# Optimization experiments

Measured on AMD Instinct MI355X. Metric: run time of the kernel, lower is better.

The kernel has to match this reference:

```python
import jax, jax.numpy as jnp
import numpy as np

N_NODES = 50000
N_EDGES = 800000
IN_FEAT = 256
OUT_FEAT = 128
P_EDGE = 0.2   # edge dropout rate
P_NODE = 0.1   # node-feature dropout rate
BN_EPS = 1e-5


def setup_inputs() -> dict:
    key = jax.random.key(0)
    ks = jax.random.split(key, 8)
    features = jax.random.normal(ks[0], (N_NODES, IN_FEAT), dtype=jnp.float32)
    W = jax.random.normal(ks[1], (IN_FEAT, OUT_FEAT), dtype=jnp.float32) / np.sqrt(IN_FEAT)
    b = jnp.zeros((OUT_FEAT,), dtype=jnp.float32)
    gamma = jnp.ones((OUT_FEAT,), dtype=jnp.float32)
    beta = jnp.zeros((OUT_FEAT,), dtype=jnp.float32)
    src = jax.random.randint(ks[2], (N_EDGES,), 0, N_NODES, dtype=jnp.int64)
    dst = jax.random.randint(ks[3], (N_EDGES,), 0, N_NODES, dtype=jnp.int64)
    edge_rand = jax.random.uniform(ks[4], (N_EDGES,), dtype=jnp.float32)
    node_rand = jax.random.uniform(ks[5], (N_NODES, OUT_FEAT), dtype=jnp.float32)
    return {"features": features, "W": W, "b": b, "gamma": gamma, "beta": beta,
            "src": src, "dst": dst, "edge_rand": edge_rand, "node_rand": node_rand}


def reference(features, W, b, gamma, beta, src, dst, edge_rand, node_rand):
    dt = features.dtype
    # --- edge dropout: keep-mask over edges (no rescale, per DropEdge convention) ---
    emask = (edge_rand >= P_EDGE).astype(dt)                      # [E]
    # --- GCN conv, norm='both' on the dropped graph ---
    h = features @ W                                              # [N, out] (W first: out < in)
    deg_src = jax.ops.segment_sum(emask, src, num_segments=N_NODES)  # out-degrees
    deg_dst = jax.ops.segment_sum(emask, dst, num_segments=N_NODES)  # in-degrees
    coef = emask * jax.lax.rsqrt(jnp.maximum(deg_src[src], 1.0) * jnp.maximum(deg_dst[dst], 1.0))
    msg = h[src] * coef[:, None]                                  # [E, out]
    agg = jax.ops.segment_sum(msg, dst, num_segments=N_NODES) + b  # [N, out]
    # --- BatchNorm1d (training mode: batch statistics over nodes) ---
    mean = jnp.mean(agg, axis=0)
    var = jnp.var(agg, axis=0)
    y = (agg - mean) * jax.lax.rsqrt(var + BN_EPS) * gamma + beta
    # --- node-feature dropout (inverted scaling) ---
    nmask = (node_rand >= P_NODE).astype(dt) / (1.0 - P_NODE)
    return y * nmask
```

## Files before the change

kernel.cpp:

```cpp
#include <hip/hip_runtime.h>

#define N_NODES 50000
#define N_EDGES 800000
#define IN_FEAT 256
#define OUT_FEAT 128
#define P_EDGE 0.2f
#define P_NODE 0.1f
#define BN_EPS 1e-5f
#define CAP 64
#define NPART 8
#define PART_N 6250
#define ECHUNKS 128
#define CHUNK_E 6250
#define GEMM_BLOCKS 782
#define ZERO_BLOCKS 98
#define PREPW_BLOCKS 128
#define AGG_BLOCKS 1024
#define FIN_BLOCKS 8

typedef __bf16 bf16x8 __attribute__((ext_vector_type(8)));
typedef float floatx4 __attribute__((ext_vector_type(4)));

__device__ inline float bflo(unsigned u) { return __uint_as_float(u << 16); }
__device__ inline float bfhi(unsigned u) { return __uint_as_float(u & 0xffff0000u); }

__global__ __launch_bounds__(256) void k_init(const float* __restrict__ W,
    uint4* __restrict__ zero_base, __bf16* __restrict__ Wt) {
  if (blockIdx.x < ZERO_BLOCKS) {
    int i = blockIdx.x * 256 + threadIdx.x;
    if (i < 25000) zero_base[i] = make_uint4(0u, 0u, 0u, 0u);
  } else {
    int idx = (blockIdx.x - ZERO_BLOCKS) * 256 + threadIdx.x;
    int k = idx >> 7, n = idx & 127;
    Wt[n * IN_FEAT + k] = (__bf16)W[idx];
  }
}

__global__ __launch_bounds__(256) void k_edge(const int* __restrict__ src,
    const int* __restrict__ dst, const float* __restrict__ er,
    unsigned* __restrict__ deg_src, unsigned* __restrict__ deg_dst,
    unsigned short* __restrict__ edge_src) {
  const int part = blockIdx.x & (NPART - 1);
  const int chunk = blockIdx.x >> 3;
  const int nlo = part * PART_N;
  const int nhi = nlo + PART_N;
  const int e0 = chunk * CHUNK_E;
  for (int e = e0 + threadIdx.x; e < e0 + CHUNK_E; e += 256) {
    if (er[e] >= P_EDGE) {
      int s = src[e], d = dst[e];
      if (s >= nlo && s < nhi) atomicAdd(&deg_src[s], 1u);
      if (d >= nlo && d < nhi) {
        unsigned p = atomicAdd(&deg_dst[d], 1u);
        if (p < CAP) edge_src[(unsigned)d * CAP + p] = (unsigned short)s;
      }
    }
  }
}

__device__ inline bf16x8 cvt8(float4 a, float4 b) {
  bf16x8 v;
  v[0] = (__bf16)a.x; v[1] = (__bf16)a.y; v[2] = (__bf16)a.z; v[3] = (__bf16)a.w;
  v[4] = (__bf16)b.x; v[5] = (__bf16)b.y; v[6] = (__bf16)b.z; v[7] = (__bf16)b.w;
  return v;
}

__global__ __launch_bounds__(256) void k_gemm(const float* __restrict__ feat,
    const __bf16* __restrict__ Wt, const unsigned* __restrict__ deg_src,
    __bf16* __restrict__ h) {
  const int lane = threadIdx.x & 63;
  const int wave = threadIdx.x >> 6;
  const int l16 = lane & 15;
  const int quad = lane >> 4;
  const int m0 = blockIdx.x * 64 + wave * 16;

  int mload = m0 + l16;
  if (mload >= N_NODES) mload = N_NODES - 1;

  bf16x8 a[8];
#pragma unroll
  for (int kk = 0; kk < 8; kk++) {
    const float4* p = (const float4*)(feat + (size_t)mload * IN_FEAT + kk * 32 + quad * 8);
    float4 f0 = p[0];
    float4 f1 = p[1];
    a[kk] = cvt8(f0, f1);
  }

  floatx4 acc[8];
#pragma unroll
  for (int g = 0; g < 8; g++) {
    const __bf16* wrow = Wt + (size_t)(g * 16 + l16) * IN_FEAT + quad * 8;
    floatx4 c = {0.f, 0.f, 0.f, 0.f};
#pragma unroll
    for (int kk = 0; kk < 8; kk++) {
      bf16x8 b = *(const bf16x8*)(wrow + kk * 32);
      c = __builtin_amdgcn_mfma_f32_16x16x32_bf16(a[kk], b, c, 0, 0, 0);
    }
    acc[g] = c;
  }

  const int rbase = m0 + quad * 4;
  float s[4];
#pragma unroll
  for (int r = 0; r < 4; r++) {
    int row = rbase + r;
    unsigned dg = (row < N_NODES) ? deg_src[row] : 1u;
    s[r] = rsqrtf((float)(dg ? dg : 1u));
  }
#pragma unroll
  for (int g = 0; g < 8; g++) {
#pragma unroll
    for (int r = 0; r < 4; r++) {
      int row = rbase + r;
      if (row < N_NODES)
        h[(size_t)row * OUT_FEAT + g * 16 + l16] = (__bf16)(acc[g][r] * s[r]);
    }
  }
}

__global__ __launch_bounds__(256) void k_agg(const unsigned short* __restrict__ h,
    const unsigned short* __restrict__ edge_src,
    const unsigned* __restrict__ deg_dst, const float* __restrict__ bias,
    float* __restrict__ out, float* __restrict__ psum, float* __restrict__ pssq) {
  const int wid = threadIdx.x >> 6;
  const int lane = threadIdx.x & 63;
  const int g = lane >> 4;
  const int cl = lane & 15;
  const int wave_global = blockIdx.x * 4 + wid;

  float b8[8];
#pragma unroll
  for (int j = 0; j < 8; j++) b8[j] = bias[cl * 8 + j];

  float s8[8], ss8[8];
#pragma unroll
  for (int j = 0; j < 8; j++) { s8[j] = 0.f; ss8[j] = 0.f; }

  unsigned cnt = deg_dst[wave_global];
  for (int d = wave_global; d < N_NODES; d += AGG_BLOCKS * 4) {
    int dn = d + AGG_BLOCKS * 4;
    unsigned cnt_next = (dn < N_NODES) ? deg_dst[dn] : 0u;
    unsigned lim = cnt > CAP ? CAP : cnt;
    const unsigned base = (unsigned)d * CAP;
    float acc[8];
#pragma unroll
    for (int j = 0; j < 8; j++) acc[j] = 0.f;

#pragma unroll 2
    for (unsigned i = 0; i < lim; i += 4) {
      unsigned e = i + (unsigned)g;
      bool valid = e < lim;
      unsigned idx = edge_src[base + (valid ? e : 0u)];
      float m = valid ? 1.f : 0.f;
      uint4 u = *(const uint4*)(h + (size_t)idx * OUT_FEAT + cl * 8);
      acc[0] = fmaf(bflo(u.x), m, acc[0]);
      acc[1] = fmaf(bfhi(u.x), m, acc[1]);
      acc[2] = fmaf(bflo(u.y), m, acc[2]);
      acc[3] = fmaf(bfhi(u.y), m, acc[3]);
      acc[4] = fmaf(bflo(u.z), m, acc[4]);
      acc[5] = fmaf(bfhi(u.z), m, acc[5]);
      acc[6] = fmaf(bflo(u.w), m, acc[6]);
      acc[7] = fmaf(bfhi(u.w), m, acc[7]);
    }
#pragma unroll
    for (int j = 0; j < 8; j++) {
      acc[j] += __shfl_xor(acc[j], 16);
      acc[j] += __shfl_xor(acc[j], 32);
    }
    if (g == 0) {
      float sc = rsqrtf((float)(cnt ? cnt : 1u));
      float o[8];
#pragma unroll
      for (int j = 0; j < 8; j++) {
        o[j] = fmaf(acc[j], sc, b8[j]);
        s8[j] += o[j];
        ss8[j] = fmaf(o[j], o[j], ss8[j]);
      }
      float4 o0 = make_float4(o[0], o[1], o[2], o[3]);
      float4 o1 = make_float4(o[4], o[5], o[6], o[7]);
      *(float4*)(out + (size_t)d * OUT_FEAT + cl * 8) = o0;
      *(float4*)(out + (size_t)d * OUT_FEAT + cl * 8 + 4) = o1;
    }
    cnt = cnt_next;
  }

  __shared__ float ls[4][16][8], lss[4][16][8];
  if (g == 0) {
#pragma unroll
    for (int j = 0; j < 8; j++) { ls[wid][cl][j] = s8[j]; lss[wid][cl][j] = ss8[j]; }
  }
  __syncthreads();
  if (threadIdx.x < 128) {
    int pcl = threadIdx.x >> 3, pj = threadIdx.x & 7;
    float t = ls[0][pcl][pj] + ls[1][pcl][pj] + ls[2][pcl][pj] + ls[3][pcl][pj];
    float t2 = lss[0][pcl][pj] + lss[1][pcl][pj] + lss[2][pcl][pj] + lss[3][pcl][pj];
    psum[blockIdx.x * OUT_FEAT + threadIdx.x] = t;
    pssq[blockIdx.x * OUT_FEAT + threadIdx.x] = t2;
  }
}

__global__ __launch_bounds__(256) void k_fin(const float* __restrict__ psum,
    const float* __restrict__ pssq, const float* __restrict__ gamma,
    const float* __restrict__ beta, float* __restrict__ a_coef,
    float* __restrict__ b_coef) {
  const int col16 = threadIdx.x & 15;
  const int slice = threadIdx.x >> 4;
  const int c = blockIdx.x * 16 + col16;
  float t = 0.f, t2 = 0.f;
  for (int b = slice; b < AGG_BLOCKS; b += 16) {
    t += psum[b * OUT_FEAT + c];
    t2 += pssq[b * OUT_FEAT + c];
  }
  __shared__ float S[16][17], S2[16][17];
  S[slice][col16] = t;
  S2[slice][col16] = t2;
  __syncthreads();
  if (threadIdx.x < 16) {
    float ts = 0.f, tss = 0.f;
#pragma unroll
    for (int s = 0; s < 16; s++) { ts += S[s][threadIdx.x]; tss += S2[s][threadIdx.x]; }
    int cc = blockIdx.x * 16 + threadIdx.x;
    float mean = ts * (1.0f / N_NODES);
    float var = tss * (1.0f / N_NODES) - mean * mean;
    float a = gamma[cc] * rsqrtf(var + BN_EPS);
    a_coef[cc] = a;
    b_coef[cc] = fmaf(-mean, a, beta[cc]);
  }
}

__global__ __launch_bounds__(256) void k_norm(float* __restrict__ out,
    const float* __restrict__ node_rand, const float* __restrict__ a_coef,
    const float* __restrict__ b_coef) {
  const size_t total4 = (size_t)N_NODES * OUT_FEAT / 4;
  size_t i = (size_t)blockIdx.x * 256 + threadIdx.x;
  if (i < total4) {
    int c0 = (int)((i * 4) & 127);
    float4 v = ((const float4*)out)[i];
    float4 nr = ((const float4*)node_rand)[i];
    float4 a = *(const float4*)(a_coef + c0);
    float4 b = *(const float4*)(b_coef + c0);
    const float inv = 1.0f / (1.0f - P_NODE);
    float4 o;
    o.x = (nr.x >= P_NODE ? inv : 0.f) * fmaf(v.x, a.x, b.x);
    o.y = (nr.y >= P_NODE ? inv : 0.f) * fmaf(v.y, a.y, b.y);
    o.z = (nr.z >= P_NODE ? inv : 0.f) * fmaf(v.z, a.z, b.z);
    o.w = (nr.w >= P_NODE ? inv : 0.f) * fmaf(v.w, a.w, b.w);
    ((float4*)out)[i] = o;
  }
}

extern "C" void kernel_launch(void* const* d_in, const int* in_sizes, int n_in,
                              void* d_out, int out_size, void* d_ws, size_t ws_size,
                              hipStream_t stream) {
  const float* feat  = (const float*)d_in[0];
  const float* W     = (const float*)d_in[1];
  const float* bias  = (const float*)d_in[2];
  const float* gamma = (const float*)d_in[3];
  const float* beta  = (const float*)d_in[4];
  const int*   src   = (const int*)d_in[5];
  const int*   dst   = (const int*)d_in[6];
  const float* er    = (const float*)d_in[7];
  const float* nr    = (const float*)d_in[8];
  float* out = (float*)d_out;

  char* ws = (char*)d_ws;
  __bf16*         h        = (__bf16*)        (ws + 0);
  unsigned short* edge_src = (unsigned short*)(ws + 12800000);
  __bf16*         Wt       = (__bf16*)        (ws + 19200000);
  unsigned*       deg_src  = (unsigned*)      (ws + 19265536);
  unsigned*       deg_dst  = (unsigned*)      (ws + 19465536);
  float*          psum     = (float*)         (ws + 19665536);
  float*          pssq     = (float*)         (ws + 20189824);
  float*          a_coef   = (float*)         (ws + 20714112);
  float*          b_coef   = (float*)         (ws + 20714624);

  k_init<<<ZERO_BLOCKS + PREPW_BLOCKS, 256, 0, stream>>>(
      W, (uint4*)(ws + 19265536), Wt);
  k_edge<<<ECHUNKS * NPART, 256, 0, stream>>>(src, dst, er, deg_src, deg_dst, edge_src);
  k_gemm<<<GEMM_BLOCKS, 256, 0, stream>>>(feat, Wt, deg_src, h);
  k_agg<<<AGG_BLOCKS, 256, 0, stream>>>((const unsigned short*)h, edge_src,
      deg_dst, bias, out, psum, pssq);
  k_fin<<<FIN_BLOCKS, 256, 0, stream>>>(psum, pssq, gamma, beta, a_coef, b_coef);
  k_norm<<<(N_NODES * OUT_FEAT / 4 + 255) / 256, 256, 0, stream>>>(out, nr, a_coef, b_coef);
}
```

Baseline: 290.9 us.

## Replace global-atomic edge bucketing with LDS counting, scan and scatter passes

The single edge pass that did global atomics on degree arrays and slot counters is split into three kernels. A count kernel builds per-chunk, per-partition histograms with packed 16-bit LDS atomics, a scan kernel turns them into per-chunk base offsets and degrees, and a scatter kernel assigns slots with LDS atomics seeded from those bases. This removes contended global atomics and the zeroing pass, at the cost of two extra launches, a second read of the edge arrays, and extra workspace for the histograms. The new buffers overlap the psum region, but they are consumed before psum is written.

```diff
diff --git a/kernel.cpp b/kernel.cpp
--- a/kernel.cpp
+++ b/kernel.cpp
@@ -10,10 +10,10 @@
 #define CAP 64
 #define NPART 8
 #define PART_N 6250
-#define ECHUNKS 128
-#define CHUNK_E 6250
+#define PWORDS 3125
+#define CCHUNK 32
+#define CHUNK_E 25000
 #define GEMM_BLOCKS 782
-#define ZERO_BLOCKS 98
 #define PREPW_BLOCKS 128
 #define AGG_BLOCKS 1024
 #define FIN_BLOCKS 8
@@ -25,33 +25,71 @@
 __device__ inline float bfhi(unsigned u) { return __uint_as_float(u & 0xffff0000u); }
 
 __global__ __launch_bounds__(256) void k_init(const float* __restrict__ W,
-    uint4* __restrict__ zero_base, __bf16* __restrict__ Wt) {
-  if (blockIdx.x < ZERO_BLOCKS) {
-    int i = blockIdx.x * 256 + threadIdx.x;
-    if (i < 25000) zero_base[i] = make_uint4(0u, 0u, 0u, 0u);
-  } else {
-    int idx = (blockIdx.x - ZERO_BLOCKS) * 256 + threadIdx.x;
-    int k = idx >> 7, n = idx & 127;
-    Wt[n * IN_FEAT + k] = (__bf16)W[idx];
-  }
-}
-
-__global__ __launch_bounds__(256) void k_edge(const int* __restrict__ src,
+    __bf16* __restrict__ Wt) {
+  int idx = blockIdx.x * 256 + threadIdx.x;
+  int k = idx >> 7, n = idx & 127;
+  Wt[n * IN_FEAT + k] = (__bf16)W[idx];
+}
+
+__global__ __launch_bounds__(256) void k_count(const int* __restrict__ src,
     const int* __restrict__ dst, const float* __restrict__ er,
-    unsigned* __restrict__ deg_src, unsigned* __restrict__ deg_dst,
-    unsigned short* __restrict__ edge_src) {
+    unsigned short* __restrict__ csrc, unsigned short* __restrict__ cdst) {
+  __shared__ unsigned s_src[PWORDS], s_dst[PWORDS];
+  const int part = blockIdx.x & (NPART - 1);
+  const int chunk = blockIdx.x >> 3;
+  for (int i = threadIdx.x; i < PWORDS; i += 256) { s_src[i] = 0u; s_dst[i] = 0u; }
+  __syncthreads();
+  const int nlo = part * PART_N;
+  const int e0 = chunk * CHUNK_E;
+  for (int e = e0 + threadIdx.x; e < e0 + CHUNK_E; e += 256) {
+    if (er[e] >= P_EDGE) {
+      int s = src[e] - nlo, d = dst[e] - nlo;
+      if ((unsigned)s < PART_N) atomicAdd(&s_src[s >> 1], 1u << ((s & 1) * 16));
+      if ((unsigned)d < PART_N) atomicAdd(&s_dst[d >> 1], 1u << ((d & 1) * 16));
+    }
+  }
+  __syncthreads();
+  unsigned* po = (unsigned*)(csrc + (size_t)chunk * N_NODES + nlo);
+  unsigned* qo = (unsigned*)(cdst + (size_t)chunk * N_NODES + nlo);
+  for (int i = threadIdx.x; i < PWORDS; i += 256) { po[i] = s_src[i]; qo[i] = s_dst[i]; }
+}
+
+__global__ __launch_bounds__(256) void k_scan(const unsigned short* __restrict__ csrc,
+    const unsigned short* __restrict__ cdst, unsigned short* __restrict__ sbase,
+    unsigned* __restrict__ deg_src, unsigned* __restrict__ deg_dst) {
+  int d = blockIdx.x * 256 + threadIdx.x;
+  if (d >= N_NODES) return;
+  unsigned ssum = 0, dsum = 0;
+#pragma unroll 8
+  for (int c = 0; c < CCHUNK; c++) {
+    ssum += csrc[(size_t)c * N_NODES + d];
+    sbase[(size_t)c * N_NODES + d] = (unsigned short)dsum;
+    dsum += cdst[(size_t)c * N_NODES + d];
+  }
+  deg_src[d] = ssum;
+  deg_dst[d] = dsum;
+}
+
+__global__ __launch_bounds__(256) void k_scatter(const int* __restrict__ src,
+    const int* __restrict__ dst, const float* __restrict__ er,
+    const unsigned short* __restrict__ sbase, unsigned short* __restrict__ edge_src) {
+  __shared__ unsigned cur[PWORDS];
   const int part = blockIdx.x & (NPART - 1);
   const int chunk = blockIdx.x >> 3;
   const int nlo = part * PART_N;
-  const int nhi = nlo + PART_N;
+  const unsigned* sb = (const unsigned*)(sbase + (size_t)chunk * N_NODES + nlo);
+  for (int i = threadIdx.x; i < PWORDS; i += 256) cur[i] = sb[i];
+  __syncthreads();
   const int e0 = chunk * CHUNK_E;
   for (int e = e0 + threadIdx.x; e < e0 + CHUNK_E; e += 256) {
     if (er[e] >= P_EDGE) {
-      int s = src[e], d = dst[e];
-      if (s >= nlo && s < nhi) atomicAdd(&deg_src[s], 1u);
-      if (d >= nlo && d < nhi) {
-        unsigned p = atomicAdd(&deg_dst[d], 1u);
-        if (p < CAP) edge_src[(unsigned)d * CAP + p] = (unsigned short)s;
+      int d = dst[e] - nlo;
+      if ((unsigned)d < PART_N) {
+        int sh = (d & 1) * 16;
+        unsigned old = atomicAdd(&cur[d >> 1], 1u << sh);
+        unsigned slot = (old >> sh) & 0xffffu;
+        if (slot < CAP)
+          edge_src[(size_t)(d + nlo) * CAP + slot] = (unsigned short)src[e];
       }
     }
   }
@@ -268,14 +306,18 @@
   __bf16*         Wt       = (__bf16*)        (ws + 19200000);
   unsigned*       deg_src  = (unsigned*)      (ws + 19265536);
   unsigned*       deg_dst  = (unsigned*)      (ws + 19465536);
+  unsigned short* csrc     = (unsigned short*)(ws + 19665536);
+  unsigned short* cdst     = (unsigned short*)(ws + 22865536);
+  unsigned short* sbase    = (unsigned short*)(ws + 26065536);
   float*          psum     = (float*)         (ws + 19665536);
   float*          pssq     = (float*)         (ws + 20189824);
   float*          a_coef   = (float*)         (ws + 20714112);
   float*          b_coef   = (float*)         (ws + 20714624);
 
-  k_init<<<ZERO_BLOCKS + PREPW_BLOCKS, 256, 0, stream>>>(
-      W, (uint4*)(ws + 19265536), Wt);
-  k_edge<<<ECHUNKS * NPART, 256, 0, stream>>>(src, dst, er, deg_src, deg_dst, edge_src);
+  k_init<<<PREPW_BLOCKS, 256, 0, stream>>>(W, Wt);
+  k_count<<<CCHUNK * NPART, 256, 0, stream>>>(src, dst, er, csrc, cdst);
+  k_scan<<<(N_NODES + 255) / 256, 256, 0, stream>>>(csrc, cdst, sbase, deg_src, deg_dst);
+  k_scatter<<<CCHUNK * NPART, 256, 0, stream>>>(src, dst, er, sbase, edge_src);
   k_gemm<<<GEMM_BLOCKS, 256, 0, stream>>>(feat, Wt, deg_src, h);
   k_agg<<<AGG_BLOCKS, 256, 0, stream>>>((const unsigned short*)h, edge_src,
       deg_dst, bias, out, psum, pssq);
```

Measured after the change: 402.6 us. 38.4% more time.
